# Performance work log

Hardware: AMD Instinct MI355X
Metric: run time of the kernel (lower is better)

Reference implementation:

```python
import jax, jax.numpy as jnp
import numpy as np
from jax import lax

B, T, N, H, OUT, FLEN = 8, 64, 512, 256, 512, 24
NEG_INF = -9.0e15


def setup_inputs() -> dict:
    key = jax.random.key(0)
    ks = jax.random.split(key, 14)
    sN = 1.0 / np.sqrt(N)
    sH = 1.0 / np.sqrt(H)
    sO = 1.0 / np.sqrt(OUT)
    return {
        "x": jax.random.normal(ks[0], (B, T, N), jnp.float32),
        "adj": jnp.ones((N, N), jnp.float32),
        "gat_W": jax.random.normal(ks[1], (1, 1), jnp.float32),
        "gat_a": jax.random.normal(ks[2], (2, 1), jnp.float32),
        "enc_Wih": jax.random.normal(ks[3], (4 * H, N), jnp.float32) * sN,
        "enc_Whh": jax.random.normal(ks[4], (4 * H, H), jnp.float32) * sH,
        "enc_bih": jax.random.normal(ks[5], (4 * H,), jnp.float32) * sH,
        "enc_bhh": jax.random.normal(ks[6], (4 * H,), jnp.float32) * sH,
        "dec_Wih": jax.random.normal(ks[7], (4 * H, OUT), jnp.float32) * sO,
        "dec_Whh": jax.random.normal(ks[8], (4 * H, H), jnp.float32) * sH,
        "dec_bih": jax.random.normal(ks[9], (4 * H,), jnp.float32) * sH,
        "dec_bhh": jax.random.normal(ks[10], (4 * H,), jnp.float32) * sH,
        "fc_W": jax.random.normal(ks[11], (OUT, H), jnp.float32) * sH,
        "fc_b": jax.random.normal(ks[12], (OUT,), jnp.float32) * sH,
    }


def _lstm_step(h, c, xt, Wih, Whh, b):
    # PyTorch gate order: i, f, g, o
    g = xt @ Wih.T + h @ Whh.T + b
    i, f, gg, o = jnp.split(g, 4, axis=-1)
    c = jax.nn.sigmoid(f) * c + jax.nn.sigmoid(i) * jnp.tanh(gg)
    h = jax.nn.sigmoid(o) * jnp.tanh(c)
    return h, c


def reference(x, adj, gat_W, gat_a, enc_Wih, enc_Whh, enc_bih, enc_bhh,
              dec_Wih, dec_Whh, dec_bih, dec_bhh, fc_W, fc_b):
    # ---- GAT over all timesteps at once (1 scalar feature per node) ----
    # Wh[b,t,n] = x[b,t,n] * W  (W is 1x1)
    f = x * gat_W[0, 0]  # [B,T,N]
    # e[b,t,i,j] = leakyrelu(a0*Wh_i + a1*Wh_j)  (cat([Wh_i,Wh_j]) @ a)
    e = jax.nn.leaky_relu(gat_a[0, 0] * f[..., :, None] + gat_a[1, 0] * f[..., None, :],
                          negative_slope=0.2)  # [B,T,N,N]
    e = jnp.where(adj > 0, e, jnp.float32(NEG_INF))
    attn = jax.nn.softmax(e, axis=-1)  # softmax over neighbors j
    x_gnn = jax.nn.relu(jnp.einsum('btij,btj->bti', attn, f))  # [B,T,N]

    # ---- LSTM encoder (scan over time) ----
    enc_b = enc_bih + enc_bhh
    def enc_step(carry, xt):
        h, c = carry
        h, c = _lstm_step(h, c, xt, enc_Wih, enc_Whh, enc_b)
        return (h, c), None
    h0 = jnp.zeros((x.shape[0], H), x.dtype)
    (h, c), _ = lax.scan(enc_step, (h0, h0), jnp.swapaxes(x_gnn, 0, 1))

    # ---- LSTMCell decoder, feeding back predictions ----
    dec_b = dec_bih + dec_bhh
    def dec_step(carry, _):
        h, c, dinp = carry
        h, c = _lstm_step(h, c, dinp, dec_Wih, dec_Whh, dec_b)
        pred = h @ fc_W.T + fc_b
        return (h, c, pred), pred
    dinp0 = jnp.zeros((x.shape[0], OUT), x.dtype)
    _, outs = lax.scan(dec_step, (h, c, dinp0), None, length=FLEN)
    return jnp.swapaxes(outs, 0, 1)  # [B, FLEN, OUT]
```

## Files before the change

kernel.cpp:

```cpp
#include <hip/hip_runtime.h>
#include <math.h>

#define Bz 8
#define Tz 64
#define Nz 512
#define Hz 256
#define OUTz 512
#define FLENz 24
#define G4H 1024
#define NBLK 256
#define NREC 64
#define NHELP 192
#define TAG_XG 7777u
#define TAG_PRE 9999u
#define TAG_WP 5555u

typedef unsigned long long u64;
typedef float f32x4 __attribute__((ext_vector_type(4)));

__device__ __forceinline__ float sigmf(float x) { return 1.f / (1.f + __expf(-x)); }

__device__ __forceinline__ void bload2(const u64* p, u64& v) {
    asm volatile("global_load_dwordx2 %0, %1, off sc0 sc1" : "=v"(v) : "v"(p));
}
__device__ __forceinline__ u64 pload(const u64* p) {
    return __hip_atomic_load(p, __ATOMIC_RELAXED, __HIP_MEMORY_SCOPE_AGENT);
}
__device__ __forceinline__ void pstore(u64* p, u64 v) {
    __hip_atomic_store(p, v, __ATOMIC_RELAXED, __HIP_MEMORY_SCOPE_AGENT);
}
__device__ __forceinline__ u64 pack(float v, unsigned tag) {
    return (u64)__float_as_uint(v) | ((u64)tag << 32);
}
__device__ __forceinline__ float pval(u64 p) { return __uint_as_float((unsigned)p); }
__device__ __forceinline__ unsigned ptag(u64 p) { return (unsigned)(p >> 32); }

__device__ void gat_one(int bt, const float* __restrict__ x, float w, float A0, float A1,
                        u64* __restrict__ xgp, float* sF, float* sR) {
    const int tid = threadIdx.x;
    const float* xr = x + (size_t)bt * Nz;
    for (int j = tid; j < Nz; j += 256) sF[j] = xr[j] * w;
    __syncthreads();
    float c0 = (A1 >= 0.f) ? fmaxf(sF[tid], sF[tid + 256]) : fminf(sF[tid], sF[tid + 256]);
    sR[tid] = c0;
    __syncthreads();
    for (int s2 = 128; s2 >= 1; s2 >>= 1) {
        if (tid < s2)
            sR[tid] = (A1 >= 0.f) ? fmaxf(sR[tid], sR[tid + s2]) : fminf(sR[tid], sR[tid + s2]);
        __syncthreads();
    }
    const float fstar = sR[0];
    const float4* f4 = (const float4*)sF;
    for (int i = tid; i < Nz; i += 256) {
        float u = A0 * sF[i];
        float zm = fmaf(A1, fstar, u);
        float m = zm > 0.f ? zm : 0.2f * zm;
        float s = 0.f, acc = 0.f;
#pragma unroll 4
        for (int jq = 0; jq < Nz / 4; ++jq) {
            float4 fj = f4[jq];
            float z0 = fmaf(A1, fj.x, u), z1 = fmaf(A1, fj.y, u);
            float z2 = fmaf(A1, fj.z, u), z3 = fmaf(A1, fj.w, u);
            z0 = z0 > 0.f ? z0 : 0.2f * z0;
            z1 = z1 > 0.f ? z1 : 0.2f * z1;
            z2 = z2 > 0.f ? z2 : 0.2f * z2;
            z3 = z3 > 0.f ? z3 : 0.2f * z3;
            float p0 = __expf(z0 - m), p1 = __expf(z1 - m);
            float p2 = __expf(z2 - m), p3 = __expf(z3 - m);
            s += p0 + p1 + p2 + p3;
            acc = fmaf(p0, fj.x, acc);
            acc = fmaf(p1, fj.y, acc);
            acc = fmaf(p2, fj.z, acc);
            acc = fmaf(p3, fj.w, acc);
        }
        pstore(xgp + (size_t)bt * Nz + i, pack(fmaxf(acc / s, 0.f), TAG_XG));
    }
    __syncthreads();
}

__device__ void pre_tile(int tc, int rc, int b,
                         const float* __restrict__ eWih,
                         const float* __restrict__ ebih,
                         const float* __restrict__ ebhh,
                         u64* __restrict__ xgp, u64* __restrict__ prep,
                         float* sXg, float* sWt) {
    const int tid = threadIdx.x;
    const int bt0 = (b * 4 + tc) * 16;
    const int r0 = rc * 128;
    __syncthreads();
    for (;;) {
        int ok = 1;
        for (int g = 0; g < 4; ++g) {
            u64 pk[8];
#pragma unroll
            for (int j = 0; j < 8; ++j)
                bload2(xgp + (size_t)bt0 * Nz + (g * 8 + j) * 256 + tid, pk[j]);
            asm volatile("s_waitcnt vmcnt(0)"
                         : "+v"(pk[0]), "+v"(pk[1]), "+v"(pk[2]), "+v"(pk[3]),
                           "+v"(pk[4]), "+v"(pk[5]), "+v"(pk[6]), "+v"(pk[7])
                         :: "memory");
#pragma unroll
            for (int j = 0; j < 8; ++j) {
                ok &= (ptag(pk[j]) == TAG_XG);
                sXg[(g * 8 + j) * 256 + tid] = pval(pk[j]);
            }
        }
        if (__syncthreads_and(ok)) break;
    }
    int r = tid & 127, bh = tid >> 7;
    int row = r0 + r;
    float bias = ebih[row] + ebhh[row];
    float acc[8];
#pragma unroll
    for (int q = 0; q < 8; ++q) acc[q] = bias;
    for (int kc = 0; kc < 16; ++kc) {
        __syncthreads();
#pragma unroll
        for (int jj = 0; jj < 16; ++jj) {
            int idx = tid + jj * 256;
            int rr = idx >> 5, kk2 = idx & 31;
            sWt[rr * 33 + kk2] = eWih[(size_t)(r0 + rr) * Nz + kc * 32 + kk2];
        }
        __syncthreads();
#pragma unroll 4
        for (int k = 0; k < 32; ++k) {
            float wv = sWt[r * 33 + k];
#pragma unroll
            for (int q = 0; q < 8; ++q)
                acc[q] = fmaf(wv, sXg[(bh * 8 + q) * Nz + kc * 32 + k], acc[q]);
        }
    }
#pragma unroll
    for (int q = 0; q < 8; ++q)
        pstore(prep + (size_t)(bt0 + bh * 8 + q) * G4H + row, pack(acc[q], TAG_PRE));
}

__global__ __launch_bounds__(256, 1) void fused_kernel(
    const float* __restrict__ x,
    const float* __restrict__ gat_W,
    const float* __restrict__ gat_a,
    const float* __restrict__ eWih,
    const float* __restrict__ eWhh,
    const float* __restrict__ ebih,
    const float* __restrict__ ebhh,
    const float* __restrict__ dWih,
    const float* __restrict__ dWhh,
    const float* __restrict__ dbih,
    const float* __restrict__ dbhh,
    const float* __restrict__ fcW,
    const float* __restrict__ fcb,
    float* __restrict__ out,
    u64* __restrict__ hp,
    u64* __restrict__ xgp,
    u64* __restrict__ prep,
    u64* __restrict__ wpq,
    u64* __restrict__ bpq)
{
    __shared__ float SM[12416];
    __shared__ float sV[256];
    __shared__ float sPs[256];
    __shared__ float sGv[128];
    __shared__ float sCst[32];
    __shared__ float sB0[128];
    __shared__ float sBp[128];
    __shared__ float sFb[64];

    const int tid = threadIdx.x;
    const int blk = blockIdx.x;
    const float w = gat_W[0], A0 = gat_a[0], A1 = gat_a[1];

    if (blk >= NREC) {
        const int hid = blk - NREC;
        for (int i = hid; i < 384; i += NHELP) {
            int t = i >> 3, b = i & 7;
            gat_one(b * 64 + t, x, w, A0, A1, xgp, SM, SM + 512);
        }
        for (int i = hid; i < 256; i += NHELP) {
            int tc = i >> 6, rem = i & 63;
            pre_tile(tc, rem >> 3, rem & 7, eWih, ebih, ebhh, xgp, prep, SM, SM + 8192);
        }
        if (hid < 128) {
            float* sDW = SM;
            float* sFcb = SM + 4096;
            int r0 = hid * 8;
            __syncthreads();
            for (int i = tid; i < 8 * OUTz; i += 256)
                sDW[i] = dWih[(size_t)r0 * OUTz + i];
            for (int i = tid; i < OUTz; i += 256) sFcb[i] = fcb[i];
            float acc[8];
#pragma unroll
            for (int rl = 0; rl < 8; ++rl)
                acc[rl] = dWhh[(size_t)(r0 + rl) * Hz + tid];
            __syncthreads();
#pragma unroll 4
            for (int o2 = 0; o2 < OUTz; ++o2) {
                float fv = fcW[(size_t)o2 * Hz + tid];
#pragma unroll
                for (int rl = 0; rl < 8; ++rl)
                    acc[rl] = fmaf(sDW[rl * OUTz + o2], fv, acc[rl]);
            }
#pragma unroll
            for (int rl = 0; rl < 8; ++rl)
                pstore(wpq + (size_t)(r0 + rl) * Hz + tid, pack(acc[rl], TAG_WP));
            if (tid < 8) {
                float s = dbih[r0 + tid] + dbhh[r0 + tid];
                for (int o2 = 0; o2 < OUTz; ++o2)
                    s = fmaf(sDW[tid * OUTz + o2], sFcb[o2], s);
                pstore(bpq + r0 + tid, pack(s, TAG_WP));
            }
        }
        return;
    }

    const int g = blk >> 3, s = blk & 7;

    gat_one((384 + blk) % 8 * 64 + ((384 + blk) >> 3), x, w, A0, A1, xgp, SM, SM + 512);
    gat_one((448 + blk) % 8 * 64 + ((448 + blk) >> 3), x, w, A0, A1, xgp, SM, SM + 512);

    const int rl = tid & 127;
    const int ks = tid >> 7;
    const int grow = ((rl >> 5) << 8) + s * 32 + (rl & 31);
    u64* hq = hp + (size_t)g * 512;

    float wReg[128];
    {
        const float* src = eWhh + (size_t)grow * Hz + ks * 128;
#pragma unroll
        for (int q = 0; q < 32; ++q)
            *(f32x4*)&wReg[q * 4] = *(const f32x4*)(src + q * 4);
    }
    float fcReg[64];
    {
        int jl = tid & 63, k4 = tid >> 6;
        const float* src = fcW + (size_t)(s * 64 + jl) * Hz + k4 * 64;
#pragma unroll
        for (int q = 0; q < 16; ++q)
            *(f32x4*)&fcReg[q * 4] = *(const f32x4*)(src + q * 4);
    }
    if (tid < 128) sB0[tid] = dbih[grow] + dbhh[grow];
    if (tid < 64) sFb[tid] = fcb[s * 64 + tid];
    if (tid < 32) sCst[tid] = 0.f;
    sV[tid] = 0.f;
    __syncthreads();

    auto partials = [&]() {
        const float* hv = &sV[ks * 128];
        float a = 0.f;
#pragma unroll
        for (int k = 0; k < 128; ++k) a = fmaf(wReg[k], hv[k], a);
        sPs[rl * 2 + ks] = a;
    };
    auto cell_store = [&](unsigned step) {
        if (tid < 32) {
            float ig = sGv[tid], fg = sGv[32 + tid], gg = sGv[64 + tid], og = sGv[96 + tid];
            float c0 = sCst[tid];
            float cn = sigmf(fg) * c0 + sigmf(ig) * tanhf(gg);
            float hn = sigmf(og) * tanhf(cn);
            sCst[tid] = cn;
            pstore(hq + (size_t)(step & 1) * 256 + s * 32 + tid, pack(hn, step + 1));
        }
    };
    auto restage = [&](unsigned step) {
        const u64* src = hq + (size_t)(step & 1) * 256 + tid;
        u64 hk;
        for (;;) {
            hk = pload(src);
            if (__syncthreads_and(ptag(hk) == step + 1)) break;
        }
        sV[tid] = pval(hk);
        __syncthreads();
    };

    for (int t = 0; t < Tz; ++t) {
        const u64* psrc = prep + ((size_t)(g * Tz + t)) * G4H + grow;
        u64 ppk = 0;
        if (tid < 128) bload2(psrc, ppk);
        partials();
        asm volatile("s_waitcnt vmcnt(0)" : "+v"(ppk) :: "memory");
        for (;;) {
            int ok = (tid < 128) ? (ptag(ppk) == TAG_PRE) : 1;
            if (__syncthreads_and(ok)) break;
            if (tid < 128) {
                bload2(psrc, ppk);
                asm volatile("s_waitcnt vmcnt(0)" : "+v"(ppk) :: "memory");
            }
        }
        if (tid < 128) sGv[tid] = pval(ppk) + sPs[tid * 2] + sPs[tid * 2 + 1];
        __syncthreads();
        cell_store(t);
        restage(t);
    }

    {
        const float* src = dWhh + (size_t)grow * Hz + ks * 128;
#pragma unroll
        for (int q = 0; q < 32; ++q)
            *(f32x4*)&wReg[q * 4] = *(const f32x4*)(src + q * 4);
        u64 bk = 0;
        for (;;) {
            int ok = 1;
            if (tid < 128) { bk = pload(bpq + grow); ok = (ptag(bk) == TAG_WP); }
            if (__syncthreads_and(ok)) break;
        }
        if (tid < 128) sBp[tid] = pval(bk);
        __syncthreads();
    }

    for (int t = 0; t < FLENz; ++t) {
        const unsigned step = Tz + t;
        partials();
        __syncthreads();
        if (tid < 128) sGv[tid] = (t == 0 ? sB0[tid] : sBp[tid]) + sPs[tid * 2] + sPs[tid * 2 + 1];
        __syncthreads();
        cell_store(step);
        restage(step);
        {
            int jl = tid & 63, k4 = tid >> 6;
            const float* hv2 = &sV[k4 * 64];
            float a2 = 0.f;
#pragma unroll
            for (int i = 0; i < 64; ++i) a2 = fmaf(fcReg[i], hv2[i], a2);
            sPs[jl * 4 + k4] = a2;
        }
        __syncthreads();
        if (tid < 64)
            out[((size_t)g * FLENz + t) * OUTz + s * 64 + tid] =
                sFb[tid] + sPs[tid * 4] + sPs[tid * 4 + 1] + sPs[tid * 4 + 2] + sPs[tid * 4 + 3];
        __syncthreads();
        if (t == 0) {
            const u64* wsrc = wpq + (size_t)grow * Hz + ks * 128;
#pragma unroll
            for (int q = 0; q < 16; ++q) {
                u64 pk8[8];
                for (;;) {
                    int ok = 1;
#pragma unroll
                    for (int j = 0; j < 8; ++j) {
                        pk8[j] = pload(wsrc + q * 8 + j);
                        ok &= (ptag(pk8[j]) == TAG_WP);
                    }
                    if (ok) break;
                }
#pragma unroll
                for (int j = 0; j < 8; ++j) wReg[q * 8 + j] = pval(pk8[j]);
            }
        }
    }
}

extern "C" void kernel_launch(void* const* d_in, const int* in_sizes, int n_in,
                              void* d_out, int out_size, void* d_ws, size_t ws_size,
                              hipStream_t stream) {
    (void)in_sizes; (void)n_in; (void)out_size; (void)ws_size;
    const float* x     = (const float*)d_in[0];
    const float* gat_W = (const float*)d_in[2];
    const float* gat_a = (const float*)d_in[3];
    const float* eWih  = (const float*)d_in[4];
    const float* eWhh  = (const float*)d_in[5];
    const float* ebih  = (const float*)d_in[6];
    const float* ebhh  = (const float*)d_in[7];
    const float* dWih  = (const float*)d_in[8];
    const float* dWhh  = (const float*)d_in[9];
    const float* dbih  = (const float*)d_in[10];
    const float* dbhh  = (const float*)d_in[11];
    const float* fcW   = (const float*)d_in[12];
    const float* fcb   = (const float*)d_in[13];
    float* out = (float*)d_out;

    u64* hp   = (u64*)d_ws;
    u64* xgp  = hp + 4096;
    u64* prep = xgp + 262144;
    u64* wpq  = prep + 524288;
    u64* bpq  = wpq + 262144;

    fused_kernel<<<NBLK, 256, 0, stream>>>(x, gat_W, gat_a, eWih, eWhh, ebih, ebhh,
                                           dWih, dWhh, dbih, dbhh, fcW, fcb,
                                           out, hp, xgp, prep, wpq, bpq);
}
```

Baseline: 426.4 us.

## Co-locate recurrent groups per XCD and exchange hidden state through L2

```diff
diff --git a/kernel.cpp b/kernel.cpp
--- a/kernel.cpp
+++ b/kernel.cpp
@@ -14,6 +14,8 @@
 #define TAG_XG 7777u
 #define TAG_PRE 9999u
 #define TAG_WP 5555u
+#define TAG_GID 3333u
+#define PZ32 0xAAAAAAAAu
 
 typedef unsigned long long u64;
 typedef float f32x4 __attribute__((ext_vector_type(4)));
@@ -23,11 +25,26 @@
 __device__ __forceinline__ void bload2(const u64* p, u64& v) {
     asm volatile("global_load_dwordx2 %0, %1, off sc0 sc1" : "=v"(v) : "v"(p));
 }
+__device__ __forceinline__ u64 sysload(const u64* p) {
+    u64 v;
+    asm volatile("global_load_dwordx2 %0, %1, off sc0 sc1\n\ts_waitcnt vmcnt(0)"
+                 : "=v"(v) : "v"(p) : "memory");
+    return v;
+}
 __device__ __forceinline__ u64 pload(const u64* p) {
     return __hip_atomic_load(p, __ATOMIC_RELAXED, __HIP_MEMORY_SCOPE_AGENT);
 }
 __device__ __forceinline__ void pstore(u64* p, u64 v) {
     __hip_atomic_store(p, v, __ATOMIC_RELAXED, __HIP_MEMORY_SCOPE_AGENT);
+}
+__device__ __forceinline__ u64 l2load(const u64* p) {
+    u64 v;
+    asm volatile("global_load_dwordx2 %0, %1, off sc0\n\ts_waitcnt vmcnt(0)"
+                 : "=v"(v) : "v"(p) : "memory");
+    return v;
+}
+__device__ __forceinline__ void l2store(u64* p, u64 v) {
+    asm volatile("global_store_dwordx2 %0, %1, off sc0" :: "v"(p), "v"(v) : "memory");
 }
 __device__ __forceinline__ u64 pack(float v, unsigned tag) {
     return (u64)__float_as_uint(v) | ((u64)tag << 32);
@@ -154,23 +171,64 @@
     u64* __restrict__ xgp,
     u64* __restrict__ prep,
     u64* __restrict__ wpq,
-    u64* __restrict__ bpq)
+    u64* __restrict__ bpq,
+    u64* __restrict__ tg,
+    unsigned* __restrict__ c32)
 {
     __shared__ float SM[12416];
     __shared__ float sV[256];
     __shared__ float sPs[256];
-    __shared__ float sGv[128];
+    __shared__ float sFc[256];
+    __shared__ float sPrep[128];
     __shared__ float sCst[32];
     __shared__ float sB0[128];
     __shared__ float sBp[128];
     __shared__ float sFb[64];
+    __shared__ int sRole[3];
 
     const int tid = threadIdx.x;
-    const int blk = blockIdx.x;
     const float w = gat_W[0], A0 = gat_a[0], A1 = gat_a[1];
 
-    if (blk >= NREC) {
-        const int hid = blk - NREC;
+    if (tid == 0) {
+        int xcd = __builtin_amdgcn_s_getreg(63508) & 7;
+        unsigned r = __hip_atomic_fetch_add(&c32[xcd], 1u, __ATOMIC_RELAXED,
+                                            __HIP_MEMORY_SCOPE_AGENT) - PZ32;
+        __hip_atomic_fetch_add(&c32[10], 1u, __ATOMIC_RELEASE, __HIP_MEMORY_SCOPE_AGENT);
+        int team = (int)(r >> 3), slot = (int)(r & 7);
+        int group = 1000;
+        if (team < 8) {
+            u64* tslot = tg + xcd * 8 + team;
+            if (slot == 7) {
+                unsigned gg = __hip_atomic_fetch_add(&c32[8], 1u, __ATOMIC_RELAXED,
+                                                     __HIP_MEMORY_SCOPE_AGENT) - PZ32;
+                pstore(tslot, (u64)gg | ((u64)TAG_GID << 32));
+                group = (int)gg;
+            } else {
+                for (;;) {
+                    u64 pk = pload(tslot);
+                    if (ptag(pk) == TAG_GID) { group = (int)(unsigned)pk; break; }
+                    unsigned tot = __hip_atomic_load(&c32[10], __ATOMIC_ACQUIRE,
+                                                     __HIP_MEMORY_SCOPE_AGENT) - PZ32;
+                    if (tot >= 256u) {
+                        unsigned cnt = __hip_atomic_load(&c32[xcd], __ATOMIC_RELAXED,
+                                                         __HIP_MEMORY_SCOPE_AGENT) - PZ32;
+                        if (cnt < (unsigned)((team + 1) * 8)) break;
+                    }
+                }
+            }
+        }
+        if (group < 8) { sRole[0] = group; sRole[1] = slot; sRole[2] = -1; }
+        else {
+            sRole[0] = -1; sRole[1] = 0;
+            sRole[2] = (int)(__hip_atomic_fetch_add(&c32[9], 1u, __ATOMIC_RELAXED,
+                                                    __HIP_MEMORY_SCOPE_AGENT) - PZ32);
+        }
+    }
+    __syncthreads();
+    const int group = sRole[0];
+
+    if (group < 0) {
+        const int hid = sRole[2];
         for (int i = hid; i < 384; i += NHELP) {
             int t = i >> 3, b = i & 7;
             gat_one(b * 64 + t, x, w, A0, A1, xgp, SM, SM + 512);
@@ -189,33 +247,34 @@
             for (int i = tid; i < OUTz; i += 256) sFcb[i] = fcb[i];
             float acc[8];
 #pragma unroll
-            for (int rl = 0; rl < 8; ++rl)
-                acc[rl] = dWhh[(size_t)(r0 + rl) * Hz + tid];
+            for (int rlq = 0; rlq < 8; ++rlq)
+                acc[rlq] = dWhh[(size_t)(r0 + rlq) * Hz + tid];
             __syncthreads();
 #pragma unroll 4
             for (int o2 = 0; o2 < OUTz; ++o2) {
                 float fv = fcW[(size_t)o2 * Hz + tid];
 #pragma unroll
-                for (int rl = 0; rl < 8; ++rl)
-                    acc[rl] = fmaf(sDW[rl * OUTz + o2], fv, acc[rl]);
+                for (int rlq = 0; rlq < 8; ++rlq)
+                    acc[rlq] = fmaf(sDW[rlq * OUTz + o2], fv, acc[rlq]);
             }
 #pragma unroll
-            for (int rl = 0; rl < 8; ++rl)
-                pstore(wpq + (size_t)(r0 + rl) * Hz + tid, pack(acc[rl], TAG_WP));
+            for (int rlq = 0; rlq < 8; ++rlq)
+                pstore(wpq + (size_t)(r0 + rlq) * Hz + tid, pack(acc[rlq], TAG_WP));
             if (tid < 8) {
-                float s = dbih[r0 + tid] + dbhh[r0 + tid];
+                float sacc = dbih[r0 + tid] + dbhh[r0 + tid];
                 for (int o2 = 0; o2 < OUTz; ++o2)
-                    s = fmaf(sDW[tid * OUTz + o2], sFcb[o2], s);
-                pstore(bpq + r0 + tid, pack(s, TAG_WP));
+                    sacc = fmaf(sDW[tid * OUTz + o2], sFcb[o2], sacc);
+                pstore(bpq + r0 + tid, pack(sacc, TAG_WP));
             }
         }
         return;
     }
 
-    const int g = blk >> 3, s = blk & 7;
-
-    gat_one((384 + blk) % 8 * 64 + ((384 + blk) >> 3), x, w, A0, A1, xgp, SM, SM + 512);
-    gat_one((448 + blk) % 8 * 64 + ((448 + blk) >> 3), x, w, A0, A1, xgp, SM, SM + 512);
+    const int g = group, s = sRole[1];
+    const int ri = g * 8 + s;
+
+    gat_one((384 + ri) % 8 * 64 + ((384 + ri) >> 3), x, w, A0, A1, xgp, SM, SM + 512);
+    gat_one((448 + ri) % 8 * 64 + ((448 + ri) >> 3), x, w, A0, A1, xgp, SM, SM + 512);
 
     const int rl = tid & 127;
     const int ks = tid >> 7;
@@ -245,50 +304,59 @@
 
     auto partials = [&]() {
         const float* hv = &sV[ks * 128];
-        float a = 0.f;
-#pragma unroll
-        for (int k = 0; k < 128; ++k) a = fmaf(wReg[k], hv[k], a);
-        sPs[rl * 2 + ks] = a;
+        float a0 = 0.f, a1 = 0.f, a2 = 0.f, a3 = 0.f;
+#pragma unroll
+        for (int k = 0; k < 128; k += 4) {
+            a0 = fmaf(wReg[k], hv[k], a0);
+            a1 = fmaf(wReg[k + 1], hv[k + 1], a1);
+            a2 = fmaf(wReg[k + 2], hv[k + 2], a2);
+            a3 = fmaf(wReg[k + 3], hv[k + 3], a3);
+        }
+        sPs[rl * 2 + ks] = (a0 + a1) + (a2 + a3);
     };
-    auto cell_store = [&](unsigned step) {
+    auto cell_store = [&](unsigned step, const float* gadd) {
         if (tid < 32) {
-            float ig = sGv[tid], fg = sGv[32 + tid], gg = sGv[64 + tid], og = sGv[96 + tid];
+            float ig = gadd[tid] + sPs[2 * tid] + sPs[2 * tid + 1];
+            float fg = gadd[32 + tid] + sPs[2 * (32 + tid)] + sPs[2 * (32 + tid) + 1];
+            float gg = gadd[64 + tid] + sPs[2 * (64 + tid)] + sPs[2 * (64 + tid) + 1];
+            float og = gadd[96 + tid] + sPs[2 * (96 + tid)] + sPs[2 * (96 + tid) + 1];
             float c0 = sCst[tid];
             float cn = sigmf(fg) * c0 + sigmf(ig) * tanhf(gg);
             float hn = sigmf(og) * tanhf(cn);
             sCst[tid] = cn;
-            pstore(hq + (size_t)(step & 1) * 256 + s * 32 + tid, pack(hn, step + 1));
+            u64 pk = pack(hn, step + 1);
+            u64* dst = hq + (size_t)(step & 1) * 256 + s * 32 + tid;
+            pstore(dst, pk);
+            l2store(dst, pk);
         }
     };
     auto restage = [&](unsigned step) {
         const u64* src = hq + (size_t)(step & 1) * 256 + tid;
-        u64 hk;
-        for (;;) {
-            hk = pload(src);
-            if (__syncthreads_and(ptag(hk) == step + 1)) break;
+        u64 hk = l2load(src);
+        int tries = 0;
+        while (ptag(hk) != step + 1) {
+            ++tries;
+            hk = (tries >= 32) ? sysload(src) : l2load(src);
         }
         sV[tid] = pval(hk);
         __syncthreads();
     };
 
+    u64 ppk = 0;
+    if (tid < 128) bload2(prep + (size_t)(g * Tz) * G4H + grow, ppk);
     for (int t = 0; t < Tz; ++t) {
-        const u64* psrc = prep + ((size_t)(g * Tz + t)) * G4H + grow;
-        u64 ppk = 0;
-        if (tid < 128) bload2(psrc, ppk);
         partials();
-        asm volatile("s_waitcnt vmcnt(0)" : "+v"(ppk) :: "memory");
-        for (;;) {
-            int ok = (tid < 128) ? (ptag(ppk) == TAG_PRE) : 1;
-            if (__syncthreads_and(ok)) break;
-            if (tid < 128) {
-                bload2(psrc, ppk);
-                asm volatile("s_waitcnt vmcnt(0)" : "+v"(ppk) :: "memory");
-            }
-        }
-        if (tid < 128) sGv[tid] = pval(ppk) + sPs[tid * 2] + sPs[tid * 2 + 1];
-        __syncthreads();
-        cell_store(t);
-        restage(t);
+        if (tid < 128) {
+            asm volatile("s_waitcnt vmcnt(0)" : "+v"(ppk) :: "memory");
+            const u64* psrc = prep + ((size_t)(g * Tz + t)) * G4H + grow;
+            while (ptag(ppk) != TAG_PRE) ppk = sysload(psrc);
+            sPrep[tid] = pval(ppk);
+            if (t + 1 < Tz)
+                bload2(prep + ((size_t)(g * Tz + t + 1)) * G4H + grow, ppk);
+        }
+        __syncthreads();
+        cell_store((unsigned)t, sPrep);
+        restage((unsigned)t);
     }
 
     {
@@ -296,37 +364,40 @@
 #pragma unroll
         for (int q = 0; q < 32; ++q)
             *(f32x4*)&wReg[q * 4] = *(const f32x4*)(src + q * 4);
-        u64 bk = 0;
-        for (;;) {
-            int ok = 1;
-            if (tid < 128) { bk = pload(bpq + grow); ok = (ptag(bk) == TAG_WP); }
-            if (__syncthreads_and(ok)) break;
-        }
-        if (tid < 128) sBp[tid] = pval(bk);
-        __syncthreads();
-    }
+        if (tid < 128) {
+            u64 bk;
+            do { bk = pload(bpq + grow); } while (ptag(bk) != TAG_WP);
+            sBp[tid] = pval(bk);
+        }
+        __syncthreads();
+    }
+
+    auto fc_partial = [&]() {
+        int jl = tid & 63, k4 = tid >> 6;
+        const float* hv2 = &sV[k4 * 64];
+        float a0 = 0.f, a1 = 0.f, a2 = 0.f, a3 = 0.f;
+#pragma unroll
+        for (int i = 0; i < 64; i += 4) {
+            a0 = fmaf(fcReg[i], hv2[i], a0);
+            a1 = fmaf(fcReg[i + 1], hv2[i + 1], a1);
+            a2 = fmaf(fcReg[i + 2], hv2[i + 2], a2);
+            a3 = fmaf(fcReg[i + 3], hv2[i + 3], a3);
+        }
+        sFc[jl * 4 + k4] = (a0 + a1) + (a2 + a3);
+    };
 
     for (int t = 0; t < FLENz; ++t) {
         const unsigned step = Tz + t;
         partials();
-        __syncthreads();
-        if (tid < 128) sGv[tid] = (t == 0 ? sB0[tid] : sBp[tid]) + sPs[tid * 2] + sPs[tid * 2 + 1];
-        __syncthreads();
-        cell_store(step);
+        if (t > 0) fc_partial();
+        __syncthreads();
+        cell_store(step, t == 0 ? sB0 : sBp);
+        if (t > 0 && tid >= 64 && tid < 128) {
+            int j = tid - 64;
+            out[((size_t)g * FLENz + (t - 1)) * OUTz + s * 64 + j] =
+                sFb[j] + sFc[j * 4] + sFc[j * 4 + 1] + sFc[j * 4 + 2] + sFc[j * 4 + 3];
+        }
         restage(step);
-        {
-            int jl = tid & 63, k4 = tid >> 6;
-            const float* hv2 = &sV[k4 * 64];
-            float a2 = 0.f;
-#pragma unroll
-            for (int i = 0; i < 64; ++i) a2 = fmaf(fcReg[i], hv2[i], a2);
-            sPs[jl * 4 + k4] = a2;
-        }
-        __syncthreads();
-        if (tid < 64)
-            out[((size_t)g * FLENz + t) * OUTz + s * 64 + tid] =
-                sFb[tid] + sPs[tid * 4] + sPs[tid * 4 + 1] + sPs[tid * 4 + 2] + sPs[tid * 4 + 3];
-        __syncthreads();
         if (t == 0) {
             const u64* wsrc = wpq + (size_t)grow * Hz + ks * 128;
 #pragma unroll
@@ -346,6 +417,11 @@
             }
         }
     }
+    fc_partial();
+    __syncthreads();
+    if (tid < 64)
+        out[((size_t)g * FLENz + (FLENz - 1)) * OUTz + s * 64 + tid] =
+            sFb[tid] + sFc[tid * 4] + sFc[tid * 4 + 1] + sFc[tid * 4 + 2] + sFc[tid * 4 + 3];
 }
 
 extern "C" void kernel_launch(void* const* d_in, const int* in_sizes, int n_in,
@@ -372,8 +448,10 @@
     u64* prep = xgp + 262144;
     u64* wpq  = prep + 524288;
     u64* bpq  = wpq + 262144;
+    u64* tg   = bpq + 1024;
+    unsigned* c32 = (unsigned*)(tg + 64);
 
     fused_kernel<<<NBLK, 256, 0, stream>>>(x, gat_W, gat_a, eWih, eWhh, ebih, ebhh,
                                            dWih, dWhh, dbih, dbhh, fcW, fcb,
-                                           out, hp, xgp, prep, wpq, bpq);
-}
+                                           out, hp, xgp, prep, wpq, bpq, tg, c32);
+}
```

Measured after the change: 609.8 us. 1.43x slower.

## Trim barriers in recurrent loop, prefetch pre-gates, defer FC output by one step

Applied to the files above, without the earlier changes.

```diff
diff --git a/kernel.cpp b/kernel.cpp
--- a/kernel.cpp
+++ b/kernel.cpp
@@ -22,6 +22,12 @@
 
 __device__ __forceinline__ void bload2(const u64* p, u64& v) {
     asm volatile("global_load_dwordx2 %0, %1, off sc0 sc1" : "=v"(v) : "v"(p));
+}
+__device__ __forceinline__ u64 sysload(const u64* p) {
+    u64 v;
+    asm volatile("global_load_dwordx2 %0, %1, off sc0 sc1\n\ts_waitcnt vmcnt(0)"
+                 : "=v"(v) : "v"(p) : "memory");
+    return v;
 }
 __device__ __forceinline__ u64 pload(const u64* p) {
     return __hip_atomic_load(p, __ATOMIC_RELAXED, __HIP_MEMORY_SCOPE_AGENT);
@@ -159,7 +165,8 @@
     __shared__ float SM[12416];
     __shared__ float sV[256];
     __shared__ float sPs[256];
-    __shared__ float sGv[128];
+    __shared__ float sFc[256];
+    __shared__ float sPrep[128];
     __shared__ float sCst[32];
     __shared__ float sB0[128];
     __shared__ float sBp[128];
@@ -212,7 +219,7 @@
         return;
     }
 
-    const int g = blk >> 3, s = blk & 7;
+    const int g = blk & 7, s = blk >> 3;
 
     gat_one((384 + blk) % 8 * 64 + ((384 + blk) >> 3), x, w, A0, A1, xgp, SM, SM + 512);
     gat_one((448 + blk) % 8 * 64 + ((448 + blk) >> 3), x, w, A0, A1, xgp, SM, SM + 512);
@@ -245,14 +252,22 @@
 
     auto partials = [&]() {
         const float* hv = &sV[ks * 128];
-        float a = 0.f;
-#pragma unroll
-        for (int k = 0; k < 128; ++k) a = fmaf(wReg[k], hv[k], a);
-        sPs[rl * 2 + ks] = a;
+        float a0 = 0.f, a1 = 0.f, a2 = 0.f, a3 = 0.f;
+#pragma unroll
+        for (int k = 0; k < 128; k += 4) {
+            a0 = fmaf(wReg[k], hv[k], a0);
+            a1 = fmaf(wReg[k + 1], hv[k + 1], a1);
+            a2 = fmaf(wReg[k + 2], hv[k + 2], a2);
+            a3 = fmaf(wReg[k + 3], hv[k + 3], a3);
+        }
+        sPs[rl * 2 + ks] = (a0 + a1) + (a2 + a3);
     };
-    auto cell_store = [&](unsigned step) {
+    auto cell_store = [&](unsigned step, const float* gadd) {
         if (tid < 32) {
-            float ig = sGv[tid], fg = sGv[32 + tid], gg = sGv[64 + tid], og = sGv[96 + tid];
+            float ig = gadd[tid] + sPs[2 * tid] + sPs[2 * tid + 1];
+            float fg = gadd[32 + tid] + sPs[2 * (32 + tid)] + sPs[2 * (32 + tid) + 1];
+            float gg = gadd[64 + tid] + sPs[2 * (64 + tid)] + sPs[2 * (64 + tid) + 1];
+            float og = gadd[96 + tid] + sPs[2 * (96 + tid)] + sPs[2 * (96 + tid) + 1];
             float c0 = sCst[tid];
             float cn = sigmf(fg) * c0 + sigmf(ig) * tanhf(gg);
             float hn = sigmf(og) * tanhf(cn);
@@ -262,33 +277,40 @@
     };
     auto restage = [&](unsigned step) {
         const u64* src = hq + (size_t)(step & 1) * 256 + tid;
-        u64 hk;
-        for (;;) {
-            hk = pload(src);
-            if (__syncthreads_and(ptag(hk) == step + 1)) break;
-        }
+        u64 hk = sysload(src);
+        while (ptag(hk) != step + 1) hk = sysload(src);
         sV[tid] = pval(hk);
         __syncthreads();
     };
-
+    auto fc_part = [&]() {
+        int jl = tid & 63, k4 = tid >> 6;
+        const float* hv2 = &sV[k4 * 64];
+        float a0 = 0.f, a1 = 0.f, a2 = 0.f, a3 = 0.f;
+#pragma unroll
+        for (int i = 0; i < 64; i += 4) {
+            a0 = fmaf(fcReg[i], hv2[i], a0);
+            a1 = fmaf(fcReg[i + 1], hv2[i + 1], a1);
+            a2 = fmaf(fcReg[i + 2], hv2[i + 2], a2);
+            a3 = fmaf(fcReg[i + 3], hv2[i + 3], a3);
+        }
+        sFc[jl * 4 + k4] = (a0 + a1) + (a2 + a3);
+    };
+
+    u64 ppk = 0;
+    if (tid < 128) bload2(prep + (size_t)(g * Tz) * G4H + grow, ppk);
     for (int t = 0; t < Tz; ++t) {
-        const u64* psrc = prep + ((size_t)(g * Tz + t)) * G4H + grow;
-        u64 ppk = 0;
-        if (tid < 128) bload2(psrc, ppk);
         partials();
-        asm volatile("s_waitcnt vmcnt(0)" : "+v"(ppk) :: "memory");
-        for (;;) {
-            int ok = (tid < 128) ? (ptag(ppk) == TAG_PRE) : 1;
-            if (__syncthreads_and(ok)) break;
-            if (tid < 128) {
-                bload2(psrc, ppk);
-                asm volatile("s_waitcnt vmcnt(0)" : "+v"(ppk) :: "memory");
-            }
-        }
-        if (tid < 128) sGv[tid] = pval(ppk) + sPs[tid * 2] + sPs[tid * 2 + 1];
-        __syncthreads();
-        cell_store(t);
-        restage(t);
+        if (tid < 128) {
+            asm volatile("s_waitcnt vmcnt(0)" : "+v"(ppk) :: "memory");
+            const u64* psrc = prep + ((size_t)(g * Tz + t)) * G4H + grow;
+            while (ptag(ppk) != TAG_PRE) ppk = sysload(psrc);
+            sPrep[tid] = pval(ppk);
+            if (t + 1 < Tz)
+                bload2(prep + ((size_t)(g * Tz + t + 1)) * G4H + grow, ppk);
+        }
+        __syncthreads();
+        cell_store((unsigned)t, sPrep);
+        restage((unsigned)t);
     }
 
     {
@@ -296,37 +318,26 @@
 #pragma unroll
         for (int q = 0; q < 32; ++q)
             *(f32x4*)&wReg[q * 4] = *(const f32x4*)(src + q * 4);
-        u64 bk = 0;
-        for (;;) {
-            int ok = 1;
-            if (tid < 128) { bk = pload(bpq + grow); ok = (ptag(bk) == TAG_WP); }
-            if (__syncthreads_and(ok)) break;
-        }
-        if (tid < 128) sBp[tid] = pval(bk);
+        if (tid < 128) {
+            u64 bk = pload(bpq + grow);
+            while (ptag(bk) != TAG_WP) bk = pload(bpq + grow);
+            sBp[tid] = pval(bk);
+        }
         __syncthreads();
     }
 
     for (int t = 0; t < FLENz; ++t) {
         const unsigned step = Tz + t;
         partials();
-        __syncthreads();
-        if (tid < 128) sGv[tid] = (t == 0 ? sB0[tid] : sBp[tid]) + sPs[tid * 2] + sPs[tid * 2 + 1];
-        __syncthreads();
-        cell_store(step);
+        if (t > 0) fc_part();
+        __syncthreads();
+        cell_store(step, t == 0 ? sB0 : sBp);
+        if (t > 0 && tid >= 64 && tid < 128) {
+            int j = tid - 64;
+            out[((size_t)g * FLENz + (t - 1)) * OUTz + s * 64 + j] =
+                sFb[j] + sFc[j * 4] + sFc[j * 4 + 1] + sFc[j * 4 + 2] + sFc[j * 4 + 3];
+        }
         restage(step);
-        {
-            int jl = tid & 63, k4 = tid >> 6;
-            const float* hv2 = &sV[k4 * 64];
-            float a2 = 0.f;
-#pragma unroll
-            for (int i = 0; i < 64; ++i) a2 = fmaf(fcReg[i], hv2[i], a2);
-            sPs[jl * 4 + k4] = a2;
-        }
-        __syncthreads();
-        if (tid < 64)
-            out[((size_t)g * FLENz + t) * OUTz + s * 64 + tid] =
-                sFb[tid] + sPs[tid * 4] + sPs[tid * 4 + 1] + sPs[tid * 4 + 2] + sPs[tid * 4 + 3];
-        __syncthreads();
         if (t == 0) {
             const u64* wsrc = wpq + (size_t)grow * Hz + ks * 128;
 #pragma unroll
@@ -346,6 +357,11 @@
             }
         }
     }
+    fc_part();
+    __syncthreads();
+    if (tid < 64)
+        out[((size_t)g * FLENz + (FLENz - 1)) * OUTz + s * 64 + tid] =
+            sFb[tid] + sFc[tid * 4] + sFc[tid * 4 + 1] + sFc[tid * 4 + 2] + sFc[tid * 4 + 3];
 }
 
 extern "C" void kernel_launch(void* const* d_in, const int* in_sizes, int n_in,
```

New measurement: 356.7 us. 16.4% less time.
